# Kernel tuning notes

Measured on AMD Instinct MI355X. Metric: run time of the kernel, lower is better.

The kernel has to match this reference:

```python
import jax, jax.numpy as jnp
import numpy as np

B, S, D, H = 2, 2048, 1024, 16
HD = D // H  # 64

def setup_inputs() -> dict:
    key = jax.random.key(0)
    ks = jax.random.split(key, 6)
    s = 1.0 / np.sqrt(D)
    return {
        "x": jax.random.normal(ks[0], (B, S, D), dtype=jnp.float32),
        "wq": jax.random.normal(ks[1], (D, D), dtype=jnp.float32) * s,
        "wk": jax.random.normal(ks[2], (D, D), dtype=jnp.float32) * s,
        "wv": jax.random.normal(ks[3], (D, D), dtype=jnp.float32) * s,
        "wo": jax.random.normal(ks[4], (D, D), dtype=jnp.float32) * s,
        "bo": jax.random.normal(ks[5], (D,), dtype=jnp.float32) * 0.01,
    }

def reference(x, wq, wk, wv, wo, bo):
    b, s, _ = x.shape
    # QKV projections (qkvBias=False), reshape to [b, h, s, hd]
    q = (x @ wq).reshape(b, s, H, HD).transpose(0, 2, 1, 3)
    k = (x @ wk).reshape(b, s, H, HD).transpose(0, 2, 1, 3)
    v = (x @ wv).reshape(b, s, H, HD).transpose(0, 2, 1, 3)
    # scores, causal mask (upper triangle -> -inf), scale, softmax
    scores = jnp.einsum('bhqd,bhkd->bhqk', q, k)
    causal = jnp.triu(jnp.ones((s, s), dtype=bool), k=1)
    scores = jnp.where(causal, -jnp.inf, scores) / np.sqrt(HD)
    weights = jax.nn.softmax(scores, axis=-1)  # dropout=0 (eval)
    ctx = jnp.einsum('bhqk,bhkd->bhqd', weights, v)
    ctx = ctx.transpose(0, 2, 1, 3).reshape(b, s, D)
    return ctx @ wo + bo
```

## Files before the change

kernel.cpp:

```cpp
#include <hip/hip_runtime.h>
#include <hip/hip_bf16.h>
#include <math.h>

#define BB 2
#define SS 2048
#define DD 1024
#define HH 16
#define HDIM 64

typedef unsigned short u16;
typedef __attribute__((ext_vector_type(8))) short bfrag;
typedef __attribute__((ext_vector_type(4))) float f32x4;

#define NEG_BIG (-1e30f)
#define QSCALE 0.18033688011112042f

__device__ __forceinline__ u16 f2u(float f) {
    unsigned int u = __builtin_bit_cast(unsigned int, f);
    u += 0x7fffu + ((u >> 16) & 1u);
    return (u16)(u >> 16);
}

__device__ __forceinline__ void async16(const u16* g, u16* l) {
    __builtin_amdgcn_global_load_lds((__attribute__((address_space(1))) void*)g,
                                     (__attribute__((address_space(3))) void*)l,
                                     16, 0, 0);
}

__device__ __forceinline__ f32x4 mfma16(bfrag a, bfrag b, f32x4 c) {
    return __builtin_amdgcn_mfma_f32_16x16x32_bf16(a, b, c, 0, 0, 0);
}

__global__ __launch_bounds__(256) void cvt_x_k(const float* __restrict__ x,
                                               u16* __restrict__ xb) {
    int i = (blockIdx.x * 256 + threadIdx.x) * 8;
    float4 a = *(const float4*)(x + i);
    float4 b = *(const float4*)(x + i + 4);
    u16 o[8] = { f2u(a.x), f2u(a.y), f2u(a.z), f2u(a.w),
                 f2u(b.x), f2u(b.y), f2u(b.z), f2u(b.w) };
    *(uint4*)(xb + i) = *(uint4*)o;
}

__global__ __launch_bounds__(256) void cvt_wT_k(const float* __restrict__ wq,
                                                const float* __restrict__ wk,
                                                const float* __restrict__ wv,
                                                const float* __restrict__ wo,
                                                u16* __restrict__ wT) {
    const float* w = (blockIdx.z == 0) ? wq : (blockIdx.z == 1) ? wk
                   : (blockIdx.z == 2) ? wv : wo;
    u16* o = wT + (size_t)blockIdx.z * DD * DD;
    __shared__ __align__(16) u16 T[64][72];
    const int t = threadIdx.x;
    const int k0 = blockIdx.x * 64, n0 = blockIdx.y * 64;
    {
        int kr = t >> 2, nb = (t & 3) * 16;
        const float4* s4 = (const float4*)(w + (size_t)(k0 + kr) * DD + n0 + nb);
        #pragma unroll
        for (int jj = 0; jj < 4; ++jj) {
            float4 v = s4[jj];
            T[kr][nb + jj*4 + 0] = f2u(v.x);
            T[kr][nb + jj*4 + 1] = f2u(v.y);
            T[kr][nb + jj*4 + 2] = f2u(v.z);
            T[kr][nb + jj*4 + 3] = f2u(v.w);
        }
    }
    __syncthreads();
    {
        int nr = t >> 2, kb = (t & 3) * 16;
        u16 tmp[16];
        #pragma unroll
        for (int j = 0; j < 16; ++j) tmp[j] = T[kb + j][nr];
        *(uint4*)(o + (size_t)(n0 + nr) * DD + k0 + kb)     = ((uint4*)tmp)[0];
        *(uint4*)(o + (size_t)(n0 + nr) * DD + k0 + kb + 8) = ((uint4*)tmp)[1];
    }
}

__global__ __launch_bounds__(256) void vtrans_k(const u16* __restrict__ V,
                                                u16* __restrict__ Vt) {
    const int bh = blockIdx.x, s0 = blockIdx.y * 64;
    const u16* src = V  + (size_t)bh * SS * HDIM;
    u16*       dst = Vt + (size_t)bh * HDIM * SS;
    __shared__ __align__(16) u16 T[64][72];
    const int t = threadIdx.x;
    {
        int sr = t >> 2, db = (t & 3) * 16;
        *(uint4*)&T[sr][db]     = *(const uint4*)(src + (size_t)(s0 + sr) * HDIM + db);
        *(uint4*)&T[sr][db + 8] = *(const uint4*)(src + (size_t)(s0 + sr) * HDIM + db + 8);
    }
    __syncthreads();
    {
        int dr = t >> 2, sb = (t & 3) * 16;
        u16 tmp[16];
        #pragma unroll
        for (int j = 0; j < 16; ++j) tmp[j] = T[sb + j][dr];
        *(uint4*)(dst + (size_t)dr * SS + s0 + sb)     = ((uint4*)tmp)[0];
        *(uint4*)(dst + (size_t)dr * SS + s0 + sb + 8) = ((uint4*)tmp)[1];
    }
}

__global__ __launch_bounds__(256) void gemm_qkv_k(
    const u16* __restrict__ xb, const u16* __restrict__ wT,
    u16* __restrict__ Qo, u16* __restrict__ Ko, u16* __restrict__ Vo)
{
    u16* out = (blockIdx.z == 0) ? Qo : (blockIdx.z == 1) ? Ko : Vo;
    const u16* wTz = wT + (size_t)blockIdx.z * DD * DD;
    const float osc = (blockIdx.z == 0) ? QSCALE : 1.0f;

    __shared__ __align__(16) u16 As[128 * 32];
    __shared__ __align__(16) u16 Bs[128 * 32];

    const int t = threadIdx.x;
    const int m0 = blockIdx.x * 128, n0 = blockIdx.y * 128;
    const int lane15 = t & 15, quad = (t >> 4) & 3, wave = t >> 6;
    const int wm = wave & 1, wn = wave >> 1;

    const int ar0 = t >> 2,        as0 = t & 3;
    const int ar1 = (t + 256) >> 2, as1 = (t + 256) & 3;
    const int ac0 = as0 ^ ((ar0 >> 1) & 3);
    const int ac1 = as1 ^ ((ar1 >> 1) & 3);
    const u16* gA0 = xb  + (size_t)(m0 + ar0) * DD + ac0 * 8;
    const u16* gA1 = xb  + (size_t)(m0 + ar1) * DD + ac1 * 8;
    const u16* gB0 = wTz + (size_t)(n0 + ar0) * DD + ac0 * 8;
    const u16* gB1 = wTz + (size_t)(n0 + ar1) * DD + ac1 * 8;
    u16* lA0 = As + (t & 192) * 8;  u16* lA1 = As + (t & 192) * 8 + 2048;
    u16* lB0 = Bs + (t & 192) * 8;  u16* lB1 = Bs + (t & 192) * 8 + 2048;

    int aoff[4], boff[4];
    #pragma unroll
    for (int mi = 0; mi < 4; ++mi) {
        int r = wm * 64 + mi * 16 + lane15;
        aoff[mi] = (r * 4 + (quad ^ ((r >> 1) & 3))) * 8;
    }
    #pragma unroll
    for (int ni = 0; ni < 4; ++ni) {
        int r = wn * 64 + ni * 16 + lane15;
        boff[ni] = (r * 4 + (quad ^ ((r >> 1) & 3))) * 8;
    }

    f32x4 acc[4][4];
    #pragma unroll
    for (int mi = 0; mi < 4; ++mi)
        #pragma unroll
        for (int ni = 0; ni < 4; ++ni)
            acc[mi][ni] = (f32x4){0.f, 0.f, 0.f, 0.f};

    for (int k0 = 0; k0 < DD; k0 += 32) {
        async16(gA0 + k0, lA0);
        async16(gA1 + k0, lA1);
        async16(gB0 + k0, lB0);
        async16(gB1 + k0, lB1);
        __syncthreads();
        bfrag av[4], bv[4];
        #pragma unroll
        for (int mi = 0; mi < 4; ++mi) av[mi] = *(const bfrag*)(As + aoff[mi]);
        #pragma unroll
        for (int ni = 0; ni < 4; ++ni) bv[ni] = *(const bfrag*)(Bs + boff[ni]);
        #pragma unroll
        for (int mi = 0; mi < 4; ++mi)
            #pragma unroll
            for (int ni = 0; ni < 4; ++ni)
                acc[mi][ni] = mfma16(av[mi], bv[ni], acc[mi][ni]);
        __syncthreads();
    }

    #pragma unroll
    for (int mi = 0; mi < 4; ++mi) {
        #pragma unroll
        for (int r = 0; r < 4; ++r) {
            int m = m0 + wm * 64 + mi * 16 + quad * 4 + r;
            int b = m >> 11, s = m & (SS - 1);
            #pragma unroll
            for (int ni = 0; ni < 4; ++ni) {
                int n = n0 + wn * 64 + ni * 16 + lane15;
                int h = n >> 6, hd = n & 63;
                out[(((size_t)(b * HH + h)) * SS + s) * HDIM + hd] = f2u(acc[mi][ni][r] * osc);
            }
        }
    }
}

__global__ __launch_bounds__(256) void gemm_out_k(
    const u16* __restrict__ ctxb, const u16* __restrict__ woT,
    const float* __restrict__ bo, float* __restrict__ out)
{
    __shared__ __align__(16) u16 As[128 * 32];
    __shared__ __align__(16) u16 Bs[64 * 32];

    const int t = threadIdx.x;
    const int m0 = blockIdx.x * 128, n0 = blockIdx.y * 64;
    const int lane15 = t & 15, quad = (t >> 4) & 3, wave = t >> 6;
    const int wm = wave & 1, wn = wave >> 1;

    const int ar0 = t >> 2,        as0 = t & 3;
    const int ar1 = (t + 256) >> 2, as1 = (t + 256) & 3;
    const int ac0 = as0 ^ ((ar0 >> 1) & 3);
    const int ac1 = as1 ^ ((ar1 >> 1) & 3);
    const u16* gA0 = ctxb + (size_t)(m0 + ar0) * DD + ac0 * 8;
    const u16* gA1 = ctxb + (size_t)(m0 + ar1) * DD + ac1 * 8;
    const u16* gB0 = woT  + (size_t)(n0 + ar0) * DD + ac0 * 8;
    u16* lA0 = As + (t & 192) * 8;  u16* lA1 = As + (t & 192) * 8 + 2048;
    u16* lB0 = Bs + (t & 192) * 8;

    int aoff[4], boff[2];
    #pragma unroll
    for (int mi = 0; mi < 4; ++mi) {
        int r = wm * 64 + mi * 16 + lane15;
        aoff[mi] = (r * 4 + (quad ^ ((r >> 1) & 3))) * 8;
    }
    #pragma unroll
    for (int ni = 0; ni < 2; ++ni) {
        int r = wn * 32 + ni * 16 + lane15;
        boff[ni] = (r * 4 + (quad ^ ((r >> 1) & 3))) * 8;
    }

    f32x4 acc[4][2];
    #pragma unroll
    for (int mi = 0; mi < 4; ++mi)
        #pragma unroll
        for (int ni = 0; ni < 2; ++ni)
            acc[mi][ni] = (f32x4){0.f, 0.f, 0.f, 0.f};

    for (int k0 = 0; k0 < DD; k0 += 32) {
        async16(gA0 + k0, lA0);
        async16(gA1 + k0, lA1);
        async16(gB0 + k0, lB0);
        __syncthreads();
        bfrag av[4], bv[2];
        #pragma unroll
        for (int mi = 0; mi < 4; ++mi) av[mi] = *(const bfrag*)(As + aoff[mi]);
        #pragma unroll
        for (int ni = 0; ni < 2; ++ni) bv[ni] = *(const bfrag*)(Bs + boff[ni]);
        #pragma unroll
        for (int mi = 0; mi < 4; ++mi)
            #pragma unroll
            for (int ni = 0; ni < 2; ++ni)
                acc[mi][ni] = mfma16(av[mi], bv[ni], acc[mi][ni]);
        __syncthreads();
    }

    float bias[2];
    #pragma unroll
    for (int ni = 0; ni < 2; ++ni)
        bias[ni] = bo[n0 + wn * 32 + ni * 16 + lane15];

    #pragma unroll
    for (int mi = 0; mi < 4; ++mi) {
        #pragma unroll
        for (int r = 0; r < 4; ++r) {
            int m = m0 + wm * 64 + mi * 16 + quad * 4 + r;
            #pragma unroll
            for (int ni = 0; ni < 2; ++ni) {
                int n = n0 + wn * 32 + ni * 16 + lane15;
                out[(size_t)m * DD + n] = acc[mi][ni][r] + bias[ni];
            }
        }
    }
}

__global__ __launch_bounds__(256) void attn_k(
    const u16* __restrict__ Q, const u16* __restrict__ K,
    const u16* __restrict__ Vt, u16* __restrict__ ctx)
{
    __shared__ __align__(16) u16 Qs[64 * 64];
    __shared__ __align__(16) u16 Ks[2][64 * 64];
    __shared__ __align__(16) u16 Vs[2][64 * 64];
    __shared__ __align__(16) u16 Ps[64 * 64];

    const int t = threadIdx.x;
    const int lane15 = t & 15, quad = (t >> 4) & 3, wave = t >> 6;
    const int bh = blockIdx.x;
    const int qt = (int)(gridDim.y - 1) - (int)blockIdx.y;
    const int q0 = qt * 64;
    const int b = bh >> 4, h = bh & 15;

    const u16* Qb = Q  + (size_t)bh * SS * HDIM;
    const u16* Kb = K  + (size_t)bh * SS * HDIM;
    const u16* Vb = Vt + (size_t)bh * HDIM * SS;

    const int kr0 = t >> 3,         ks0 = t & 7;
    const int kr1 = (t + 256) >> 3, ks1 = (t + 256) & 7;
    const int kc0 = ks0 ^ (kr0 & 7);
    const int kc1 = ks1 ^ (kr1 & 7);
    const int ldst = (t & 192) * 8;

    async16(Qb + (size_t)(q0 + kr0) * HDIM + kc0 * 8, Qs + ldst);
    async16(Qb + (size_t)(q0 + kr1) * HDIM + kc1 * 8, Qs + ldst + 2048);
    async16(Kb + (size_t)kr0 * HDIM + kc0 * 8, Ks[0] + ldst);
    async16(Kb + (size_t)kr1 * HDIM + kc1 * 8, Ks[0] + ldst + 2048);
    async16(Vb + (size_t)kr0 * SS + kc0 * 8, Vs[0] + ldst);
    async16(Vb + (size_t)kr1 * SS + kc1 * 8, Vs[0] + ldst + 2048);

    const int qrow = wave * 16 + lane15;
    int qoff[2], koff[4][2];
    #pragma unroll
    for (int kh = 0; kh < 2; ++kh)
        qoff[kh] = (qrow * 8 + ((kh * 4 + quad) ^ (qrow & 7))) * 8;
    #pragma unroll
    for (int ni = 0; ni < 4; ++ni)
        #pragma unroll
        for (int kh = 0; kh < 2; ++kh) {
            int row = ni * 16 + lane15;
            koff[ni][kh] = (row * 8 + ((kh * 4 + quad) ^ (row & 7))) * 8;
        }

    f32x4 acc_o[4];
    float rsum[4] = {0.f, 0.f, 0.f, 0.f};
    #pragma unroll
    for (int nd = 0; nd < 4; ++nd) acc_o[nd] = (f32x4){0.f, 0.f, 0.f, 0.f};

    const int qgb = q0 + wave * 16 + quad * 4;

    for (int kt = 0; kt <= qt; ++kt) {
        __syncthreads();
        if (kt < qt) {
            const int nv0 = (kt + 1) * 64;
            u16* kd = Ks[(kt + 1) & 1];
            u16* vd = Vs[(kt + 1) & 1];
            async16(Kb + (size_t)(nv0 + kr0) * HDIM + kc0 * 8, kd + ldst);
            async16(Kb + (size_t)(nv0 + kr1) * HDIM + kc1 * 8, kd + ldst + 2048);
            async16(Vb + (size_t)kr0 * SS + nv0 + kc0 * 8, vd + ldst);
            async16(Vb + (size_t)kr1 * SS + nv0 + kc1 * 8, vd + ldst + 2048);
        }
        const u16* ksb = Ks[kt & 1];
        const u16* vsb = Vs[kt & 1];
        const int kv0 = kt * 64;

        f32x4 s_acc[4];
        #pragma unroll
        for (int ni = 0; ni < 4; ++ni) s_acc[ni] = (f32x4){0.f, 0.f, 0.f, 0.f};
        #pragma unroll
        for (int kh = 0; kh < 2; ++kh) {
            bfrag aq = *(const bfrag*)(Qs + qoff[kh]);
            #pragma unroll
            for (int ni = 0; ni < 4; ++ni)
                s_acc[ni] = mfma16(aq, *(const bfrag*)(ksb + koff[ni][kh]), s_acc[ni]);
        }

        const bool diag = (kt == qt);
        #pragma unroll
        for (int ni = 0; ni < 4; ++ni) {
            int kvg = kv0 + ni * 16 + lane15;
            #pragma unroll
            for (int r = 0; r < 4; ++r) {
                float v = s_acc[ni][r];
                if (diag && (kvg > qgb + r)) v = NEG_BIG;
                float pw = exp2f(v);
                rsum[r] += pw;
                int row = wave * 16 + quad * 4 + r;
                int col = ni * 16 + lane15;
                Ps[(row * 8 + ((col >> 3) ^ (row & 7))) * 8 + (col & 7)] = f2u(pw);
            }
        }

        #pragma unroll
        for (int kh = 0; kh < 2; ++kh) {
            bfrag ap = *(const bfrag*)(Ps + qoff[kh]);
            #pragma unroll
            for (int nd = 0; nd < 4; ++nd)
                acc_o[nd] = mfma16(ap, *(const bfrag*)(vsb + koff[nd][kh]), acc_o[nd]);
        }
    }

    #pragma unroll
    for (int off = 1; off < 16; off <<= 1)
        #pragma unroll
        for (int r = 0; r < 4; ++r)
            rsum[r] += __shfl_xor(rsum[r], off, 64);

    #pragma unroll
    for (int r = 0; r < 4; ++r) {
        float inv = 1.f / rsum[r];
        int srow = q0 + wave * 16 + quad * 4 + r;
        size_t base = ((size_t)b * SS + srow) * DD + h * HDIM;
        #pragma unroll
        for (int nd = 0; nd < 4; ++nd)
            ctx[base + nd * 16 + lane15] = f2u(acc_o[nd][r] * inv);
    }
}

extern "C" void kernel_launch(void* const* d_in, const int* in_sizes, int n_in,
                              void* d_out, int out_size, void* d_ws, size_t ws_size,
                              hipStream_t stream) {
    const float* x  = (const float*)d_in[0];
    const float* wq = (const float*)d_in[1];
    const float* wk = (const float*)d_in[2];
    const float* wv = (const float*)d_in[3];
    const float* wo = (const float*)d_in[4];
    const float* bo = (const float*)d_in[5];
    float* out = (float*)d_out;

    char* ws = (char*)d_ws;
    const size_t MB8 = (size_t)8 * 1024 * 1024;
    u16* xb  = (u16*)(ws);
    u16* wT  = (u16*)(ws + MB8);
    u16* Qb  = (u16*)(ws + 2 * MB8);
    u16* Kb  = (u16*)(ws + 3 * MB8);
    u16* Vb  = (u16*)(ws + 4 * MB8);
    u16* Vt   = xb;
    u16* ctxb = Vb;

    cvt_x_k <<<2048, 256, 0, stream>>>(x, xb);
    cvt_wT_k<<<dim3(16, 16, 4), 256, 0, stream>>>(wq, wk, wv, wo, wT);
    gemm_qkv_k<<<dim3(32, 8, 3), 256, 0, stream>>>(xb, wT, Qb, Kb, Vb);
    vtrans_k<<<dim3(32, 32), 256, 0, stream>>>(Vb, Vt);
    attn_k  <<<dim3(32, 32), 256, 0, stream>>>(Qb, Kb, Vt, ctxb);
    gemm_out_k<<<dim3(32, 16), 256, 0, stream>>>(ctxb, wT + (size_t)3 * DD * DD, bo, out);
}
```

Before: 182.8 us.

## Fuse V transpose into QKV GEMM epilogue and shrink attention shared memory

The QKV GEMM now writes V directly in transposed [bh, d, s] layout through a swizzled shared-memory staging tile, so the separate vtrans kernel and its extra global round-trip are gone. In the attention kernel, Q fragments are held in registers and the Q shared buffer is reused for P. This cuts LDS use and adds a min-blocks launch bound for higher occupancy. P is now truncated rather than rounded to bf16, and the row sum uses the truncated values so normalization stays consistent. This adds barriers in the GEMM epilogue and changes the position of the loop barrier.

Result: slower. 187.0 us (+2.3%).

```diff
diff --git a/kernel.cpp b/kernel.cpp
--- a/kernel.cpp
+++ b/kernel.cpp
@@ -75,39 +75,16 @@
     }
 }
 
-__global__ __launch_bounds__(256) void vtrans_k(const u16* __restrict__ V,
-                                                u16* __restrict__ Vt) {
-    const int bh = blockIdx.x, s0 = blockIdx.y * 64;
-    const u16* src = V  + (size_t)bh * SS * HDIM;
-    u16*       dst = Vt + (size_t)bh * HDIM * SS;
-    __shared__ __align__(16) u16 T[64][72];
-    const int t = threadIdx.x;
-    {
-        int sr = t >> 2, db = (t & 3) * 16;
-        *(uint4*)&T[sr][db]     = *(const uint4*)(src + (size_t)(s0 + sr) * HDIM + db);
-        *(uint4*)&T[sr][db + 8] = *(const uint4*)(src + (size_t)(s0 + sr) * HDIM + db + 8);
-    }
-    __syncthreads();
-    {
-        int dr = t >> 2, sb = (t & 3) * 16;
-        u16 tmp[16];
-        #pragma unroll
-        for (int j = 0; j < 16; ++j) tmp[j] = T[sb + j][dr];
-        *(uint4*)(dst + (size_t)dr * SS + s0 + sb)     = ((uint4*)tmp)[0];
-        *(uint4*)(dst + (size_t)dr * SS + s0 + sb + 8) = ((uint4*)tmp)[1];
-    }
-}
-
 __global__ __launch_bounds__(256) void gemm_qkv_k(
     const u16* __restrict__ xb, const u16* __restrict__ wT,
-    u16* __restrict__ Qo, u16* __restrict__ Ko, u16* __restrict__ Vo)
+    u16* __restrict__ Qo, u16* __restrict__ Ko, u16* __restrict__ Vt)
 {
-    u16* out = (blockIdx.z == 0) ? Qo : (blockIdx.z == 1) ? Ko : Vo;
     const u16* wTz = wT + (size_t)blockIdx.z * DD * DD;
     const float osc = (blockIdx.z == 0) ? QSCALE : 1.0f;
 
-    __shared__ __align__(16) u16 As[128 * 32];
-    __shared__ __align__(16) u16 Bs[128 * 32];
+    __shared__ __align__(16) u16 smem[8192];
+    u16* As = smem;
+    u16* Bs = smem + 4096;
 
     const int t = threadIdx.x;
     const int m0 = blockIdx.x * 128, n0 = blockIdx.y * 128;
@@ -163,18 +140,53 @@
         __syncthreads();
     }
 
-    #pragma unroll
-    for (int mi = 0; mi < 4; ++mi) {
-        #pragma unroll
-        for (int r = 0; r < 4; ++r) {
-            int m = m0 + wm * 64 + mi * 16 + quad * 4 + r;
-            int b = m >> 11, s = m & (SS - 1);
-            #pragma unroll
-            for (int ni = 0; ni < 4; ++ni) {
-                int n = n0 + wn * 64 + ni * 16 + lane15;
-                int h = n >> 6, hd = n & 63;
-                out[(((size_t)(b * HH + h)) * SS + s) * HDIM + hd] = f2u(acc[mi][ni][r] * osc);
+    if (blockIdx.z != 2) {
+        u16* out = (blockIdx.z == 0) ? Qo : Ko;
+        #pragma unroll
+        for (int mi = 0; mi < 4; ++mi) {
+            #pragma unroll
+            for (int r = 0; r < 4; ++r) {
+                int m = m0 + wm * 64 + mi * 16 + quad * 4 + r;
+                int b = m >> 11, s = m & (SS - 1);
+                #pragma unroll
+                for (int ni = 0; ni < 4; ++ni) {
+                    int n = n0 + wn * 64 + ni * 16 + lane15;
+                    int h = n >> 6, hd = n & 63;
+                    out[(((size_t)(b * HH + h)) * SS + s) * HDIM + hd] = f2u(acc[mi][ni][r] * osc);
+                }
             }
+        }
+    } else {
+        u16* T = smem;
+        const int bq = m0 >> 11;
+        const int ms = m0 & (SS - 1);
+        #pragma unroll
+        for (int hh = 0; hh < 2; ++hh) {
+            if (wn == hh) {
+                #pragma unroll
+                for (int mi = 0; mi < 4; ++mi)
+                    #pragma unroll
+                    for (int r = 0; r < 4; ++r) {
+                        int ml = wm * 64 + mi * 16 + quad * 4 + r;
+                        #pragma unroll
+                        for (int ni = 0; ni < 4; ++ni) {
+                            int nl = ni * 16 + lane15;
+                            T[nl * 128 + (ml ^ ((nl & 7) << 4))] = f2u(acc[mi][ni][r]);
+                        }
+                    }
+            }
+            __syncthreads();
+            const int h = (n0 >> 6) + hh;
+            u16* dst = Vt + ((size_t)(bq * HH + h)) * (HDIM * SS);
+            #pragma unroll
+            for (int i = 0; i < 4; ++i) {
+                int c = t + i * 256;
+                int row = c >> 4;
+                int mb  = (c & 15) * 8;
+                uint4 val = *(const uint4*)&T[row * 128 + (mb ^ ((row & 7) << 4))];
+                *(uint4*)(dst + (size_t)row * SS + ms + mb) = val;
+            }
+            __syncthreads();
         }
     }
 }
@@ -257,14 +269,13 @@
     }
 }
 
-__global__ __launch_bounds__(256) void attn_k(
+__global__ __launch_bounds__(256, 4) void attn_k(
     const u16* __restrict__ Q, const u16* __restrict__ K,
     const u16* __restrict__ Vt, u16* __restrict__ ctx)
 {
-    __shared__ __align__(16) u16 Qs[64 * 64];
+    __shared__ __align__(16) u16 QP[64 * 64];
     __shared__ __align__(16) u16 Ks[2][64 * 64];
     __shared__ __align__(16) u16 Vs[2][64 * 64];
-    __shared__ __align__(16) u16 Ps[64 * 64];
 
     const int t = threadIdx.x;
     const int lane15 = t & 15, quad = (t >> 4) & 3, wave = t >> 6;
@@ -283,8 +294,8 @@
     const int kc1 = ks1 ^ (kr1 & 7);
     const int ldst = (t & 192) * 8;
 
-    async16(Qb + (size_t)(q0 + kr0) * HDIM + kc0 * 8, Qs + ldst);
-    async16(Qb + (size_t)(q0 + kr1) * HDIM + kc1 * 8, Qs + ldst + 2048);
+    async16(Qb + (size_t)(q0 + kr0) * HDIM + kc0 * 8, QP + ldst);
+    async16(Qb + (size_t)(q0 + kr1) * HDIM + kc1 * 8, QP + ldst + 2048);
     async16(Kb + (size_t)kr0 * HDIM + kc0 * 8, Ks[0] + ldst);
     async16(Kb + (size_t)kr1 * HDIM + kc1 * 8, Ks[0] + ldst + 2048);
     async16(Vb + (size_t)kr0 * SS + kc0 * 8, Vs[0] + ldst);
@@ -303,6 +314,12 @@
             koff[ni][kh] = (row * 8 + ((kh * 4 + quad) ^ (row & 7))) * 8;
         }
 
+    __syncthreads();
+    bfrag aq[2];
+    aq[0] = *(const bfrag*)(QP + qoff[0]);
+    aq[1] = *(const bfrag*)(QP + qoff[1]);
+    __syncthreads();
+
     f32x4 acc_o[4];
     float rsum[4] = {0.f, 0.f, 0.f, 0.f};
     #pragma unroll
@@ -311,7 +328,6 @@
     const int qgb = q0 + wave * 16 + quad * 4;
 
     for (int kt = 0; kt <= qt; ++kt) {
-        __syncthreads();
         if (kt < qt) {
             const int nv0 = (kt + 1) * 64;
             u16* kd = Ks[(kt + 1) & 1];
@@ -329,12 +345,10 @@
         #pragma unroll
         for (int ni = 0; ni < 4; ++ni) s_acc[ni] = (f32x4){0.f, 0.f, 0.f, 0.f};
         #pragma unroll
-        for (int kh = 0; kh < 2; ++kh) {
-            bfrag aq = *(const bfrag*)(Qs + qoff[kh]);
+        for (int kh = 0; kh < 2; ++kh)
             #pragma unroll
             for (int ni = 0; ni < 4; ++ni)
-                s_acc[ni] = mfma16(aq, *(const bfrag*)(ksb + koff[ni][kh]), s_acc[ni]);
-        }
+                s_acc[ni] = mfma16(aq[kh], *(const bfrag*)(ksb + koff[ni][kh]), s_acc[ni]);
 
         const bool diag = (kt == qt);
         #pragma unroll
@@ -345,20 +359,22 @@
                 float v = s_acc[ni][r];
                 if (diag && (kvg > qgb + r)) v = NEG_BIG;
                 float pw = exp2f(v);
-                rsum[r] += pw;
+                unsigned pu = __builtin_bit_cast(unsigned, pw);
+                rsum[r] += __builtin_bit_cast(float, pu & 0xffff0000u);
                 int row = wave * 16 + quad * 4 + r;
                 int col = ni * 16 + lane15;
-                Ps[(row * 8 + ((col >> 3) ^ (row & 7))) * 8 + (col & 7)] = f2u(pw);
+                QP[(row * 8 + ((col >> 3) ^ (row & 7))) * 8 + (col & 7)] = (u16)(pu >> 16);
             }
         }
 
         #pragma unroll
         for (int kh = 0; kh < 2; ++kh) {
-            bfrag ap = *(const bfrag*)(Ps + qoff[kh]);
+            bfrag ap = *(const bfrag*)(QP + qoff[kh]);
             #pragma unroll
             for (int nd = 0; nd < 4; ++nd)
                 acc_o[nd] = mfma16(ap, *(const bfrag*)(vsb + koff[nd][kh]), acc_o[nd]);
         }
+        __syncthreads();
     }
 
     #pragma unroll
@@ -395,14 +411,12 @@
     u16* wT  = (u16*)(ws + MB8);
     u16* Qb  = (u16*)(ws + 2 * MB8);
     u16* Kb  = (u16*)(ws + 3 * MB8);
-    u16* Vb  = (u16*)(ws + 4 * MB8);
-    u16* Vt   = xb;
-    u16* ctxb = Vb;
+    u16* Vt  = (u16*)(ws + 4 * MB8);
+    u16* ctxb = xb;
 
     cvt_x_k <<<2048, 256, 0, stream>>>(x, xb);
     cvt_wT_k<<<dim3(16, 16, 4), 256, 0, stream>>>(wq, wk, wv, wo, wT);
-    gemm_qkv_k<<<dim3(32, 8, 3), 256, 0, stream>>>(xb, wT, Qb, Kb, Vb);
-    vtrans_k<<<dim3(32, 32), 256, 0, stream>>>(Vb, Vt);
+    gemm_qkv_k<<<dim3(32, 8, 3), 256, 0, stream>>>(xb, wT, Qb, Kb, Vt);
     attn_k  <<<dim3(32, 32), 256, 0, stream>>>(Qb, Kb, Vt, ctxb);
     gemm_out_k<<<dim3(32, 16), 256, 0, stream>>>(ctxb, wT + (size_t)3 * DD * DD, bo, out);
 }
```
